# Kernel optimization log

Hardware: AMD Instinct MI355X
Metric: run time of the kernel (lower is better)

Reference implementation:

```python
import jax, jax.numpy as jnp
import numpy as np

N = 8192        # nodes
V = 50000       # vocab = len(dict_node_names)
EMB = 256       # embedding_dim
XI = EMB // 2   # x_increased_dim = 128
DIN = EMB + XI  # 384, SelfAtt_ dim
H = 4           # n_heads
D = 128         # WGAT output_dim per head (fusion dim)
E = 131072      # edges
CHUNK = 32768   # chunk_size (E % CHUNK == 0)


def _ln(x, g, b, eps=1e-5):
    m = jnp.mean(x, axis=-1, keepdims=True)
    v = jnp.mean((x - m) ** 2, axis=-1, keepdims=True)
    return (x - m) * jax.lax.rsqrt(v + eps) * g + b


def _wgat(emb, src, dst, edge_attr, wi, bi, wj, bj, wt, bt, attn):
    # x_i = features at destination (aggregation target), x_j = source/neighbor
    x_i = emb[dst]                                   # [E, din]
    x_j = emb[src]                                   # [E, din]
    h = (x_i @ wi + bi).reshape(E, H, D) + (x_j @ wj + bj).reshape(E, H, D)
    a = jnp.einsum('ehd,hd->eh', h, attn)            # [E, H]
    a = a * edge_attr[:, None]                       # edge weights pre-softmax
    # faithful chunked softmax: normalize over edges WITHIN each chunk (dim=0 per chunk)
    a = jax.nn.softmax(a.reshape(E // CHUNK, CHUNK, H), axis=1).reshape(E, H)
    xt = (x_j @ wt + bt).reshape(E, H, D)            # [E, H, D]
    msg = jnp.einsum('ehd,eh->ed', xt, a)            # sum over heads -> [E, D]
    return jax.ops.segment_sum(msg, dst, num_segments=N)  # aggr='add'


def _emb_forward(ids, edge_index, x, edge_attr, embed,
                 qkv_w, qkv_b, proj_w, proj_b, fuse_w, fuse_b, ln1_g, ln1_b,
                 wi0, bi0, wj0, bj0, wt0, bt0, attn0, skip0_w, skip0_b,
                 wi1, bi1, wj1, bj1, wt1, bt1, attn1, skip1_w, skip1_b,
                 ln2_g, ln2_b):
    E_i = embed[ids]                                 # [N, EMB] gather
    z = jnp.concatenate([jnp.tile(x, (1, XI)), E_i], axis=-1)   # [N, DIN]
    # SelfAtt_ : full N x N attention over nodes, scale = DIN**-0.5
    qkv = z @ qkv_w + qkv_b
    q, k, v = jnp.split(qkv, 3, axis=-1)
    att = jax.nn.softmax((q @ k.T) * (DIN ** -0.5), axis=-1) @ v
    z = att @ proj_w + proj_b                        # [N, DIN]
    emb = jax.nn.silu(_ln(z @ fuse_w + fuse_b, ln1_g, ln1_b)) + E_i  # [N, EMB]
    src, dst = edge_index[0], edge_index[1]
    emb = _wgat(emb, src, dst, edge_attr, wi0, bi0, wj0, bj0, wt0, bt0, attn0)  # [N, D]
    s0 = emb @ skip0_w + skip0_b
    emb = _wgat(emb, src, dst, edge_attr, wi1, bi1, wj1, bj1, wt1, bt1, attn1)  # [N, D]
    s1 = emb @ skip1_w + skip1_b
    emb = _ln(emb + (s0 + s1) * 0.5, ln2_g, ln2_b)
    return emb


def setup_inputs() -> dict:
    key = jax.random.key(0)
    ks = jax.random.split(key, 32)

    def w(k, shape, scale=0.05):
        return jax.random.normal(k, shape, jnp.float32) * scale

    inp = {}
    inp['ids'] = jax.random.randint(ks[0], (N,), 0, V)
    inp['x'] = jax.random.normal(ks[1], (N, 1), jnp.float32)
    inp['edge_attr'] = jax.random.uniform(ks[2], (E,), jnp.float32)
    inp['edge_index'] = jax.random.randint(ks[3], (2, E), 0, N)
    inp['embed'] = w(ks[4], (V, EMB), 1.0)
    inp['qkv_w'] = w(ks[5], (DIN, 3 * DIN)); inp['qkv_b'] = jnp.zeros((3 * DIN,), jnp.float32)
    inp['proj_w'] = w(ks[6], (DIN, DIN));    inp['proj_b'] = jnp.zeros((DIN,), jnp.float32)
    inp['fuse_w'] = w(ks[7], (DIN, EMB));    inp['fuse_b'] = jnp.zeros((EMB,), jnp.float32)
    inp['ln1_g'] = jnp.ones((EMB,), jnp.float32); inp['ln1_b'] = jnp.zeros((EMB,), jnp.float32)
    # WGAT layer 0: in=EMB, out=D per head, H heads
    inp['wi0'] = w(ks[8], (EMB, H * D));  inp['bi0'] = jnp.zeros((H * D,), jnp.float32)
    inp['wj0'] = w(ks[9], (EMB, H * D));  inp['bj0'] = jnp.zeros((H * D,), jnp.float32)
    inp['wt0'] = w(ks[10], (EMB, H * D)); inp['bt0'] = jnp.zeros((H * D,), jnp.float32)
    inp['attn0'] = w(ks[11], (H, D), 0.1)
    inp['skip0_w'] = w(ks[12], (D, D));   inp['skip0_b'] = jnp.zeros((D,), jnp.float32)
    # WGAT layer 1: in=D
    inp['wi1'] = w(ks[13], (D, H * D));   inp['bi1'] = jnp.zeros((H * D,), jnp.float32)
    inp['wj1'] = w(ks[14], (D, H * D));   inp['bj1'] = jnp.zeros((H * D,), jnp.float32)
    inp['wt1'] = w(ks[15], (D, H * D));   inp['bt1'] = jnp.zeros((H * D,), jnp.float32)
    inp['attn1'] = w(ks[16], (H, D), 0.1)
    inp['skip1_w'] = w(ks[17], (D, D));   inp['skip1_b'] = jnp.zeros((D,), jnp.float32)
    inp['ln2_g'] = jnp.ones((D,), jnp.float32); inp['ln2_b'] = jnp.zeros((D,), jnp.float32)
    return inp


def reference(ids, x, edge_attr, edge_index, embed,
              qkv_w, qkv_b, proj_w, proj_b, fuse_w, fuse_b, ln1_g, ln1_b,
              wi0, bi0, wj0, bj0, wt0, bt0, attn0, skip0_w, skip0_b,
              wi1, bi1, wj1, bj1, wt1, bt1, attn1, skip1_w, skip1_b,
              ln2_g, ln2_b):
    emb = _emb_forward(ids, edge_index, x, edge_attr, embed,
                       qkv_w, qkv_b, proj_w, proj_b, fuse_w, fuse_b, ln1_g, ln1_b,
                       wi0, bi0, wj0, bj0, wt0, bt0, attn0, skip0_w, skip0_b,
                       wi1, bi1, wj1, bj1, wt1, bt1, attn1, skip1_w, skip1_b,
                       ln2_g, ln2_b)
    return (emb, embed, ids)
```

## Files before the change

### kernel.cpp

```cpp
#include <hip/hip_runtime.h>

typedef __attribute__((ext_vector_type(8))) short bfrag;
typedef __attribute__((ext_vector_type(4))) float f4;

#define MFMA(a,b,c) __builtin_amdgcn_mfma_f32_16x16x32_bf16(a,b,c,0,0,0)

__device__ __forceinline__ unsigned short f2b(float x){
  union { float f; unsigned int u; } v; v.f = x;
  unsigned int r = v.u + 0x7fffu + ((v.u >> 16) & 1u);
  return (unsigned short)(r >> 16);
}
__device__ __forceinline__ float b2f(unsigned short h){
  union { unsigned int u; float f; } v; v.u = ((unsigned int)h) << 16;
  return v.f;
}

__global__ __launch_bounds__(256) void k_prep(
    const float* __restrict__ qkv_w, const float* __restrict__ proj_w,
    const float* __restrict__ fuse_w, const float* __restrict__ wt0,
    const float* __restrict__ wt1, const float* __restrict__ sk0w,
    const float* __restrict__ wi0, const float* __restrict__ bi0,
    const float* __restrict__ wj0, const float* __restrict__ bj0,
    const float* __restrict__ wi1, const float* __restrict__ bi1,
    const float* __restrict__ wj1, const float* __restrict__ bj1,
    const float* __restrict__ attn0, const float* __restrict__ attn1,
    const float* __restrict__ bt0, const float* __restrict__ bt1,
    const float* __restrict__ sk0b,
    const float* __restrict__ embed, const int* __restrict__ ids,
    unsigned short* __restrict__ BtQKV, unsigned short* __restrict__ BtPROJ,
    unsigned short* __restrict__ BtFUSE, unsigned short* __restrict__ BtT0,
    unsigned short* __restrict__ BtT1,
    float* __restrict__ biasT0, float* __restrict__ biasT1,
    float* __restrict__ wsum, float* __restrict__ Ei)
{
  int b = blockIdx.x, t = threadIdx.x;
  if (b < 1152) {
    int idx = b*256 + t; int k = idx/1152, n = idx - k*1152;
    BtQKV[(size_t)n*256 + k] = f2b(qkv_w[128*1152 + idx]);
  } else if (b < 1728) {
    int idx = (b-1152)*256 + t; int k = idx/384, n = idx - k*384;
    BtPROJ[(size_t)n*384 + k] = f2b(proj_w[idx]);
  } else if (b < 2112) {
    int idx = (b-1728)*256 + t; int k = idx/256, n = idx - k*256;
    BtFUSE[(size_t)n*384 + k] = f2b(fuse_w[idx]);
  } else if (b < 2624) {
    int idx = (b-2112)*256 + t; int k = idx/512, n = idx - k*512;
    BtT0[(size_t)n*256 + k] = f2b(wt0[idx]);
  } else if (b < 2880) {
    int idx = (b-2624)*256 + t; int k = idx/512, n = idx - k*512;
    BtT1[(size_t)n*128 + k] = f2b(wt1[idx]);
  } else if (b < 2944) {
    int idx = (b-2880)*256 + t; int k = idx/128, n = idx - k*128;
    BtT1[(size_t)(512+n)*128 + k] = f2b(sk0w[idx]);
  } else if (b < 2948) {
    int idx = (b-2944)*256 + t;
    int h = idx >> 8, k = idx & 255;
    float s = 0.f;
    for (int d = 0; d < 128; ++d) s += wi0[(size_t)k*512 + h*128 + d] * attn0[h*128 + d];
    BtT0[(size_t)(512 + h)*256 + k] = f2b(s);
    if (idx < 4) {
      float sb = 0.f;
      for (int d = 0; d < 128; ++d) sb += bi0[idx*128 + d] * attn0[idx*128 + d];
      biasT0[512 + idx] = sb;
    }
  } else if (b < 2952) {
    int idx = (b-2948)*256 + t;
    int h = idx >> 8, k = idx & 255;
    float s = 0.f;
    for (int d = 0; d < 128; ++d) s += wj0[(size_t)k*512 + h*128 + d] * attn0[h*128 + d];
    BtT0[(size_t)(516 + h)*256 + k] = f2b(s);
    if (idx < 4) {
      float sb = 0.f;
      for (int d = 0; d < 128; ++d) sb += bj0[idx*128 + d] * attn0[idx*128 + d];
      biasT0[516 + idx] = sb;
    }
  } else if (b < 2954) {
    int idx = (b-2952)*256 + t;
    int h = idx >> 7, k = idx & 127;
    float s = 0.f;
    for (int d = 0; d < 128; ++d) s += wi1[(size_t)k*512 + h*128 + d] * attn1[h*128 + d];
    BtT1[(size_t)(640 + h)*128 + k] = f2b(s);
    if (idx < 4) {
      float sb = 0.f;
      for (int d = 0; d < 128; ++d) sb += bi1[idx*128 + d] * attn1[idx*128 + d];
      biasT1[640 + idx] = sb;
    }
  } else if (b < 2956) {
    int idx = (b-2954)*256 + t;
    int h = idx >> 7, k = idx & 127;
    float s = 0.f;
    for (int d = 0; d < 128; ++d) s += wj1[(size_t)k*512 + h*128 + d] * attn1[h*128 + d];
    BtT1[(size_t)(644 + h)*128 + k] = f2b(s);
    if (idx < 4) {
      float sb = 0.f;
      for (int d = 0; d < 128; ++d) sb += bj1[idx*128 + d] * attn1[idx*128 + d];
      biasT1[644 + idx] = sb;
    }
  } else if (b < 2958) {
    int idx = (b-2956)*256 + t; biasT0[idx] = bt0[idx];
  } else if (b < 2960) {
    int idx = (b-2958)*256 + t; biasT1[idx] = bt1[idx];
  } else if (b < 2961) {
    if (t < 128) biasT1[512 + t] = sk0b[t];
  } else if (b < 2966) {
    int n = (b-2961)*256 + t;
    if (n < 1152) {
      float s = 0.f;
      for (int k = 0; k < 128; ++k) s += qkv_w[(size_t)k*1152 + n];
      wsum[n] = s;
    }
  } else {
    int idx = (b-2966)*256 + t;
    int n = idx >> 6, c4 = idx & 63;
    reinterpret_cast<float4*>(Ei)[idx] =
        reinterpret_cast<const float4*>(embed + (size_t)ids[n]*256)[c4];
  }
}

__global__ void k_outcopy(const float* __restrict__ embed, const int* __restrict__ ids,
                          float* __restrict__ out){
  int i = blockIdx.x*256 + threadIdx.x;
  if (i < 3200000)
    reinterpret_cast<float4*>(out)[262144 + i] = reinterpret_cast<const float4*>(embed)[i];
  if (i < 8192) out[13848576 + i] = (float)ids[i];
}

__global__ void k_deg(const int* __restrict__ ei, int* __restrict__ deg){
  int e = blockIdx.x*256 + threadIdx.x; if (e >= 131072) return;
  atomicAdd(&deg[ei[131072 + e]], 1);
}

__global__ __launch_bounds__(1024) void k_scan(const int* __restrict__ deg,
                                               int* __restrict__ off, int* __restrict__ cursor){
  int t = threadIdx.x;
  int v[8]; int s = 0;
  #pragma unroll
  for (int i=0;i<8;++i){ v[i] = s; s += deg[t*8 + i]; }
  int lane = t & 63, w = t >> 6;
  int si = s;
  for (int o=1;o<64;o<<=1){ int u = __shfl_up(si, o); if (lane >= o) si += u; }
  __shared__ int wsum[16];
  if (lane == 63) wsum[w] = si;
  __syncthreads();
  if (t < 16) {
    int x = wsum[t];
    for (int o=1;o<16;o<<=1){ int u = __shfl_up(x, o); if (t >= o) x += u; }
    wsum[t] = x;
  }
  __syncthreads();
  int wbase = (w == 0) ? 0 : wsum[w-1];
  int base = wbase + (si - s);
  #pragma unroll
  for (int i=0;i<8;++i){ int o2 = base + v[i]; off[t*8+i] = o2; cursor[t*8+i] = o2; }
  if (t == 1023) off[8192] = wbase + si;
}

__global__ void k_fill(const int* __restrict__ ei, int* __restrict__ cursor,
                       int* __restrict__ elist){
  int e = blockIdx.x*256 + threadIdx.x; if (e >= 131072) return;
  int d = ei[131072 + e];
  int slot = atomicAdd(&cursor[d], 1);
  elist[slot] = e;
}

__global__ __launch_bounds__(256) void k_gemm(
    const float* __restrict__ A, int lda,
    const unsigned short* __restrict__ Bt, int K,
    const float* __restrict__ bias,
    float* __restrict__ C, int ldc, int mode,
    const float* __restrict__ xv, const float* __restrict__ wsum,
    unsigned short* __restrict__ qO, unsigned short* __restrict__ kO,
    unsigned short* __restrict__ vO)
{
  __shared__ unsigned short As[128*40];
  __shared__ unsigned short Bs[128*40];
  const int t = threadIdx.x;
  const int wid = t >> 6, l = t & 63;
  const int lr = l & 15, lg = l >> 4;
  const int arow0 = blockIdx.y*128, bn0 = blockIdx.x*128;
  const int wr = (wid >> 1)*64, wc = (wid & 1)*64;
  f4 zero = {0.f,0.f,0.f,0.f};
  f4 acc[4][4];
  #pragma unroll
  for (int i=0;i<4;++i)
    #pragma unroll
    for (int j=0;j<4;++j) acc[i][j] = zero;

  for (int k0 = 0; k0 < K; k0 += 32) {
    #pragma unroll
    for (int p=0;p<4;++p) {
      int row = p*32 + (t>>3);
      int c4  = (t&7)*4;
      float4 v = *reinterpret_cast<const float4*>(A + (size_t)(arow0+row)*lda + k0 + c4);
      ushort4 h4;
      h4.x = f2b(v.x); h4.y = f2b(v.y); h4.z = f2b(v.z); h4.w = f2b(v.w);
      *reinterpret_cast<ushort4*>(&As[row*40 + c4]) = h4;
    }
    #pragma unroll
    for (int p=0;p<2;++p) {
      int n  = p*64 + (t>>2);
      int c8 = (t&3)*8;
      int4 v = *reinterpret_cast<const int4*>(Bt + (size_t)(bn0+n)*K + k0 + c8);
      *reinterpret_cast<int4*>(&Bs[n*40 + c8]) = v;
    }
    __syncthreads();
    bfrag af[4], bfm[4];
    #pragma unroll
    for (int mi=0;mi<4;++mi) af[mi] = *reinterpret_cast<const bfrag*>(&As[(wr+mi*16+lr)*40 + lg*8]);
    #pragma unroll
    for (int ni=0;ni<4;++ni) bfm[ni] = *reinterpret_cast<const bfrag*>(&Bs[(wc+ni*16+lr)*40 + lg*8]);
    #pragma unroll
    for (int mi=0;mi<4;++mi)
      #pragma unroll
      for (int ni=0;ni<4;++ni)
        acc[mi][ni] = MFMA(af[mi], bfm[ni], acc[mi][ni]);
    __syncthreads();
  }
  #pragma unroll
  for (int mi=0;mi<4;++mi) {
    #pragma unroll
    for (int ni=0;ni<4;++ni) {
      int col = bn0 + wc + ni*16 + lr;
      float bv = bias[col];
      float wsv = (mode==1) ? wsum[col] : 0.f;
      #pragma unroll
      for (int i=0;i<4;++i) {
        int row = arow0 + wr + mi*16 + lg*4 + i;
        float val = acc[mi][ni][i] + bv;
        if (mode == 1) {
          val += xv[row]*wsv;
          if (col < 384) val *= 0.05103103631f;
          unsigned short hv = f2b(val);
          if (col < 384)      qO[(size_t)row*384 + col] = hv;
          else if (col < 768) kO[(size_t)row*384 + col - 384] = hv;
          else                vO[(size_t)(col-768)*8192 + row] = hv;
        } else {
          C[(size_t)row*ldc + col] = val;
        }
      }
    }
  }
}

__global__ __launch_bounds__(256,2) void k_flash(
    const unsigned short* __restrict__ qg,
    const unsigned short* __restrict__ kg,
    const unsigned short* __restrict__ vg,
    unsigned short* __restrict__ Opart, float* __restrict__ mpart, float* __restrict__ lpart)
{
  __shared__ unsigned short Ks[32*384];
  __shared__ unsigned short Ps[64*40];
  __shared__ float m_s[64], l_s[64], f_s[64];

  const int t = threadIdx.x;
  const int w = t >> 6, l = t & 63;
  const int lr = l & 15, lg = l >> 4;
  const int qbi = blockIdx.x >> 2, split = blockIdx.x & 3;
  const int qbase = qbi * 64;

  #define STAGE(JJ) do { \
    _Pragma("unroll") \
    for (int p_=0;p_<6;++p_) { \
      int idx_ = p_*256 + t; \
      int row_ = idx_ / 48, uu_ = idx_ - row_*48; \
      int ug_ = uu_ ^ (row_ & 7); \
      const unsigned short* gp_ = kg + (size_t)((JJ) + row_)*384 + ug_*8; \
      __builtin_amdgcn_global_load_lds((const __attribute__((address_space(1))) void*)gp_, \
          (__attribute__((address_space(3))) void*)&Ks[idx_*8], 16, 0, 0); \
    } } while(0)

  bfrag qf[12];
  #pragma unroll
  for (int kk=0;kk<12;++kk)
    qf[kk] = *reinterpret_cast<const bfrag*>(qg + (size_t)(qbase + w*16 + lr)*384 + kk*32 + lg*8);

  f4 zero = {0.f,0.f,0.f,0.f};
  f4 o[4][6];
  #pragma unroll
  for (int a=0;a<4;++a)
    #pragma unroll
    for (int b=0;b<6;++b) o[a][b] = zero;

  const int j0beg = split*2048, jend = j0beg + 2048;

  STAGE(j0beg);
  if (t < 64) { m_s[t] = -3e38f; l_s[t] = 0.f; }
  __syncthreads();

  for (int j0 = j0beg; j0 < jend; j0 += 32) {
    bfrag vf[6];
    #pragma unroll
    for (int nj=0;nj<6;++nj)
      vf[nj] = *reinterpret_cast<const bfrag*>(vg + (size_t)(w*96 + nj*16 + lr)*8192 + j0 + lg*8);

    f4 s0 = zero, s1 = zero;
    __builtin_amdgcn_s_setprio(1);
    #pragma unroll
    for (int kk=0;kk<12;++kk) {
      int su = ((kk*4 + lg) ^ (lr & 7)) * 8;
      bfrag b0 = *reinterpret_cast<const bfrag*>(&Ks[lr*384 + su]);
      bfrag b1 = *reinterpret_cast<const bfrag*>(&Ks[(16+lr)*384 + su]);
      s0 = MFMA(qf[kk], b0, s0);
      s1 = MFMA(qf[kk], b1, s1);
    }
    __builtin_amdgcn_s_setprio(0);

    #pragma unroll
    for (int i=0;i<4;++i) {
      int row = w*16 + lg*4 + i;
      float mt = fmaxf(s0[i], s1[i]);
      mt = fmaxf(mt, __shfl_xor(mt, 1));
      mt = fmaxf(mt, __shfl_xor(mt, 2));
      mt = fmaxf(mt, __shfl_xor(mt, 4));
      mt = fmaxf(mt, __shfl_xor(mt, 8));
      float mo = m_s[row];
      float mn = fmaxf(mo, mt);
      float p0 = __expf(s0[i] - mn), p1 = __expf(s1[i] - mn);
      float sum = p0 + p1;
      sum += __shfl_xor(sum, 1);
      sum += __shfl_xor(sum, 2);
      sum += __shfl_xor(sum, 4);
      sum += __shfl_xor(sum, 8);
      Ps[row*40 + lr]      = f2b(p0);
      Ps[row*40 + 16 + lr] = f2b(p1);
      if (lr == 0) {
        float f = __expf(mo - mn);
        m_s[row] = mn; f_s[row] = f; l_s[row] = l_s[row]*f + sum;
      }
    }
    __syncthreads();

    if (j0 + 32 < jend) STAGE(j0 + 32);

    #pragma unroll
    for (int omi=0; omi<4; ++omi) {
      #pragma unroll
      for (int i=0;i<4;++i) {
        float f = f_s[omi*16 + lg*4 + i];
        #pragma unroll
        for (int nj=0;nj<6;++nj) o[omi][nj][i] *= f;
      }
    }
    bfrag pa[4];
    #pragma unroll
    for (int omi=0;omi<4;++omi)
      pa[omi] = *reinterpret_cast<const bfrag*>(&Ps[(omi*16+lr)*40 + lg*8]);
    __builtin_amdgcn_s_setprio(1);
    #pragma unroll
    for (int nj=0;nj<6;++nj)
      #pragma unroll
      for (int omi=0;omi<4;++omi)
        o[omi][nj] = MFMA(pa[omi], vf[nj], o[omi][nj]);
    __builtin_amdgcn_s_setprio(0);
    __syncthreads();
  }
  #undef STAGE

  unsigned short* Op = Opart + (size_t)split*8192*384;
  #pragma unroll
  for (int omi=0;omi<4;++omi)
    #pragma unroll
    for (int nj=0;nj<6;++nj)
      #pragma unroll
      for (int i=0;i<4;++i)
        Op[(size_t)(qbase + omi*16 + lg*4 + i)*384 + w*96 + nj*16 + lr] = f2b(o[omi][nj][i]);
  if (t < 64) {
    mpart[split*8192 + qbase + t] = m_s[t];
    lpart[split*8192 + qbase + t] = l_s[t];
  }
}

__global__ void k_combine(const unsigned short* __restrict__ Op, const float* __restrict__ mp,
                          const float* __restrict__ lp, float* __restrict__ att)
{
  int gid = blockIdx.x*256 + threadIdx.x;
  int row = gid / 384;
  float m0 = mp[row], m1 = mp[8192+row], m2 = mp[16384+row], m3 = mp[24576+row];
  float M = fmaxf(fmaxf(m0,m1), fmaxf(m2,m3));
  float w0 = __expf(m0-M), w1 = __expf(m1-M), w2 = __expf(m2-M), w3 = __expf(m3-M);
  float L = lp[row]*w0 + lp[8192+row]*w1 + lp[16384+row]*w2 + lp[24576+row]*w3;
  const size_t Z = (size_t)8192*384;
  float acc = b2f(Op[gid])*w0 + b2f(Op[Z+gid])*w1 + b2f(Op[2*Z+gid])*w2 + b2f(Op[3*Z+gid])*w3;
  att[gid] = acc / L;
}

__global__ __launch_bounds__(256) void k_ln1(const float* __restrict__ pre, const float* __restrict__ Ei,
                      const float* __restrict__ g, const float* __restrict__ b,
                      float* __restrict__ out)
{
  int row = blockIdx.x, c = threadIdx.x;
  float v = pre[(size_t)row*256 + c];
  float s1 = v, s2 = v*v;
  #pragma unroll
  for (int o1=32;o1;o1>>=1){ s1 += __shfl_down(s1,o1); s2 += __shfl_down(s2,o1); }
  __shared__ float a1[4], a2[4];
  if ((c&63)==0){ a1[c>>6] = s1; a2[c>>6] = s2; }
  __syncthreads();
  float S1 = a1[0]+a1[1]+a1[2]+a1[3], S2 = a2[0]+a2[1]+a2[2]+a2[3];
  float mean = S1*(1.f/256.f), var = S2*(1.f/256.f) - mean*mean;
  float y = (v-mean)*rsqrtf(var+1e-5f)*g[c] + b[c];
  float sig = 1.f/(1.f+__expf(-y));
  out[(size_t)row*256 + c] = y*sig + Ei[(size_t)row*256 + c];
}

__global__ void k_escore(const int* __restrict__ ei, const float* __restrict__ ea,
                         const float* __restrict__ TC, int ldc, int aoff,
                         float* __restrict__ sc)
{
  int e = blockIdx.x*256 + threadIdx.x; if (e >= 131072) return;
  int s = ei[e], d = ei[131072 + e];
  float wv = ea[e];
  #pragma unroll
  for (int h=0; h<4; ++h) {
    float ai = TC[(size_t)d*ldc + aoff + h];
    float aj = TC[(size_t)s*ldc + aoff + 4 + h];
    sc[e*4 + h] = (ai + aj) * wv;
  }
}

__global__ __launch_bounds__(1024) void k_cstats(const float* __restrict__ sc,
                        float* __restrict__ mx, float* __restrict__ sm)
{
  int ch = blockIdx.x;
  int c = ch >> 2, h = ch & 3;
  int t = threadIdx.x;
  const float* base = sc + (size_t)c*131072 + h;
  float m = -3e38f;
  for (int i=t; i<32768; i+=1024) m = fmaxf(m, base[(size_t)i*4]);
  #pragma unroll
  for (int o1=32;o1;o1>>=1) m = fmaxf(m, __shfl_down(m,o1));
  __shared__ float red[16];
  if ((t&63)==0) red[t>>6] = m;
  __syncthreads();
  if (t == 0) { float x = red[0]; for (int i=1;i<16;++i) x = fmaxf(x, red[i]); red[0] = x; }
  __syncthreads();
  float M = red[0];
  float s = 0.f;
  for (int i=t; i<32768; i+=1024) s += __expf(base[(size_t)i*4] - M);
  #pragma unroll
  for (int o1=32;o1;o1>>=1) s += __shfl_down(s,o1);
  __shared__ float red2[16];
  if ((t&63)==0) red2[t>>6] = s;
  __syncthreads();
  if (t == 0) { float x = 0.f; for (int i=0;i<16;++i) x += red2[i]; mx[ch] = M; sm[ch] = x; }
}

__global__ void k_pnorm(float* __restrict__ sc, const float* __restrict__ mx,
                        const float* __restrict__ sm)
{
  int i = blockIdx.x*256 + threadIdx.x;
  int e = i >> 2, h = i & 3;
  int ch = (e >> 15)*4 + h;
  sc[i] = __expf(sc[i] - mx[ch]) / sm[ch];
}

__global__ __launch_bounds__(128) void k_aggr(const int* __restrict__ off,
                      const int* __restrict__ elist, const int* __restrict__ ei,
                      const float* __restrict__ sc,
                      const float* __restrict__ TC, int ldc, float* __restrict__ g)
{
  int n = blockIdx.x, d = threadIdx.x;
  int qb = off[n], qe = off[n+1];
  float acc = 0.f;
  for (int q = qb; q < qe; ++q) {
    int e = elist[q];
    int s = ei[e];
    float4 p = *reinterpret_cast<const float4*>(&sc[e*4]);
    const float* Tr = TC + (size_t)s*ldc;
    acc += p.x*Tr[d] + p.y*Tr[128+d] + p.z*Tr[256+d] + p.w*Tr[384+d];
  }
  g[(size_t)n*128 + d] = acc;
}

__global__ __launch_bounds__(128) void k_final(const float* __restrict__ g1, const float* __restrict__ TC1,
                       const float* __restrict__ sw, const float* __restrict__ sb,
                       const float* __restrict__ lg2, const float* __restrict__ lb2,
                       float* __restrict__ out)
{
  int row = blockIdx.x, c = threadIdx.x;
  __shared__ float gr[128];
  float gv = g1[(size_t)row*128 + c];
  gr[c] = gv; __syncthreads();
  float s1 = sb[c];
  #pragma unroll 8
  for (int k=0;k<128;++k) s1 += gr[k]*sw[k*128 + c];
  float s0 = TC1[(size_t)row*768 + 512 + c];
  float v = gv + 0.5f*(s0 + s1);
  float m1 = v, m2 = v*v;
  #pragma unroll
  for (int o1=32;o1;o1>>=1){ m1 += __shfl_down(m1,o1); m2 += __shfl_down(m2,o1); }
  __shared__ float a1[2], a2[2];
  if ((c&63)==0){ a1[c>>6]=m1; a2[c>>6]=m2; }
  __syncthreads();
  float S1 = a1[0]+a1[1], S2 = a2[0]+a2[1];
  float mean = S1*(1.f/128.f), var = S2*(1.f/128.f) - mean*mean;
  out[(size_t)row*128 + c] = (v-mean)*rsqrtf(var+1e-5f)*lg2[c] + lb2[c];
}

extern "C" void kernel_launch(void* const* d_in, const int* in_sizes, int n_in,
                              void* d_out, int out_size, void* d_ws, size_t ws_size,
                              hipStream_t stream)
{
  const int*   ids    = (const int*)  d_in[0];
  const float* x      = (const float*)d_in[1];
  const float* ea     = (const float*)d_in[2];
  const int*   eidx   = (const int*)  d_in[3];
  const float* embed  = (const float*)d_in[4];
  const float* qkv_w  = (const float*)d_in[5];
  const float* qkv_b  = (const float*)d_in[6];
  const float* proj_w = (const float*)d_in[7];
  const float* proj_b = (const float*)d_in[8];
  const float* fuse_w = (const float*)d_in[9];
  const float* fuse_b = (const float*)d_in[10];
  const float* ln1_g  = (const float*)d_in[11];
  const float* ln1_b  = (const float*)d_in[12];
  const float* wi0 = (const float*)d_in[13]; const float* bi0 = (const float*)d_in[14];
  const float* wj0 = (const float*)d_in[15]; const float* bj0 = (const float*)d_in[16];
  const float* wt0 = (const float*)d_in[17]; const float* bt0 = (const float*)d_in[18];
  const float* attn0 = (const float*)d_in[19];
  const float* sk0w = (const float*)d_in[20]; const float* sk0b = (const float*)d_in[21];
  const float* wi1 = (const float*)d_in[22]; const float* bi1 = (const float*)d_in[23];
  const float* wj1 = (const float*)d_in[24]; const float* bj1 = (const float*)d_in[25];
  const float* wt1 = (const float*)d_in[26]; const float* bt1 = (const float*)d_in[27];
  const float* attn1 = (const float*)d_in[28];
  const float* sk1w = (const float*)d_in[29]; const float* sk1b = (const float*)d_in[30];
  const float* ln2_g = (const float*)d_in[31]; const float* ln2_b = (const float*)d_in[32];

  char* ws = (char*)d_ws;
  const size_t MBy = (size_t)1 << 20;

  unsigned short* BtQKV  = (unsigned short*)(ws + 0);
  unsigned short* BtPROJ = (unsigned short*)(ws + 589824);
  unsigned short* BtFUSE = (unsigned short*)(ws + 884736);
  unsigned short* BtT0   = (unsigned short*)(ws + 1081344);
  unsigned short* BtT1   = (unsigned short*)(ws + 1409024);
  float* biasT0 = (float*)(ws + 1605632);
  float* biasT1 = (float*)(ws + 1608192);
  float* wsum   = (float*)(ws + 1611264);
  float* mxb    = (float*)(ws + 1615872);
  float* smb    = (float*)(ws + 1615936);
  int* deg    = (int*)(ws + 1703936);
  int* cursor = (int*)(ws + 1736704);
  int* off    = (int*)(ws + 1769472);

  float* Ei   = (float*)(ws + 2*MBy);
  unsigned short* qb = (unsigned short*)(ws + 10*MBy);
  unsigned short* kb = (unsigned short*)(ws + 17*MBy);
  unsigned short* vb = (unsigned short*)(ws + 24*MBy);
  float* att  = (float*)(ws + 31*MBy);
  float* z2   = (float*)(ws + 10*MBy);
  float* pre  = (float*)(ws + 45*MBy);
  float* emb0 = (float*)(ws + 31*MBy);
  float* TC0  = (float*)(ws + 43*MBy);
  float* sc0  = (float*)(ws + 26*MBy);
  float* g0   = (float*)(ws + 2*MBy);
  float* TC1  = (float*)(ws + 6*MBy);
  float* sc1  = (float*)(ws + 43*MBy);
  float* g1   = (float*)(ws + 47448064);
  int* elist  = (int*)(ws + 64*MBy);

  float* out = (float*)d_out;
  unsigned short* Opart = (unsigned short*)d_out;
  float* mpart = out + 6815744;
  float* lpart = out + 6848512;

  hipMemsetAsync(ws, 0, 2*MBy, stream);

  k_prep<<<5014, 256, 0, stream>>>(qkv_w, proj_w, fuse_w, wt0, wt1, sk0w,
                                   wi0, bi0, wj0, bj0, wi1, bi1, wj1, bj1,
                                   attn0, attn1, bt0, bt1, sk0b, embed, ids,
                                   BtQKV, BtPROJ, BtFUSE, BtT0, BtT1,
                                   biasT0, biasT1, wsum, Ei);
  k_deg<<<512, 256, 0, stream>>>(eidx, deg);
  k_scan<<<1, 1024, 0, stream>>>(deg, off, cursor);
  k_fill<<<512, 256, 0, stream>>>(eidx, cursor, elist);

  k_gemm<<<dim3(9,64), 256, 0, stream>>>(Ei, 256, BtQKV, 256, qkv_b, nullptr, 0, 1,
                                         x, wsum, qb, kb, vb);
  k_flash<<<512, 256, 0, stream>>>(qb, kb, vb, Opart, mpart, lpart);
  k_combine<<<12288, 256, 0, stream>>>(Opart, mpart, lpart, att);
  k_outcopy<<<12500, 256, 0, stream>>>(embed, ids, out);

  k_gemm<<<dim3(3,64), 256, 0, stream>>>(att, 384, BtPROJ, 384, proj_b, z2, 384, 0,
                                         nullptr, nullptr, nullptr, nullptr, nullptr);
  k_gemm<<<dim3(2,64), 256, 0, stream>>>(z2, 384, BtFUSE, 384, fuse_b, pre, 256, 0,
                                         nullptr, nullptr, nullptr, nullptr, nullptr);
  k_ln1<<<8192, 256, 0, stream>>>(pre, Ei, ln1_g, ln1_b, emb0);

  k_gemm<<<dim3(5,64), 256, 0, stream>>>(emb0, 256, BtT0, 256, biasT0, TC0, 640, 0,
                                         nullptr, nullptr, nullptr, nullptr, nullptr);
  k_escore<<<512, 256, 0, stream>>>(eidx, ea, TC0, 640, 512, sc0);
  k_cstats<<<16, 1024, 0, stream>>>(sc0, mxb, smb);
  k_pnorm<<<2048, 256, 0, stream>>>(sc0, mxb, smb);
  k_aggr<<<8192, 128, 0, stream>>>(off, elist, eidx, sc0, TC0, 640, g0);

  k_gemm<<<dim3(6,64), 256, 0, stream>>>(g0, 128, BtT1, 128, biasT1, TC1, 768, 0,
                                         nullptr, nullptr, nullptr, nullptr, nullptr);
  k_escore<<<512, 256, 0, stream>>>(eidx, ea, TC1, 768, 640, sc1);
  k_cstats<<<16, 1024, 0, stream>>>(sc1, mxb, smb);
  k_pnorm<<<2048, 256, 0, stream>>>(sc1, mxb, smb);
  k_aggr<<<8192, 128, 0, stream>>>(off, elist, eidx, sc1, TC1, 768, g1);

  k_final<<<8192, 128, 0, stream>>>(g1, TC1, sk1w, sk1b, ln2_g, ln2_b, out);
}
```

Measured before the change: 526.5 us.

## Make flash-attention waves independent with register-resident softmax and direct K/V loads

```diff
diff --git a/kernel.cpp b/kernel.cpp
--- a/kernel.cpp
+++ b/kernel.cpp
@@ -2,6 +2,7 @@
 
 typedef __attribute__((ext_vector_type(8))) short bfrag;
 typedef __attribute__((ext_vector_type(4))) float f4;
+typedef __attribute__((ext_vector_type(4))) unsigned int ui4;
 
 #define MFMA(a,b,c) __builtin_amdgcn_mfma_f32_16x16x32_bf16(a,b,c,0,0,0)
 
@@ -248,125 +249,105 @@
     const unsigned short* __restrict__ vg,
     unsigned short* __restrict__ Opart, float* __restrict__ mpart, float* __restrict__ lpart)
 {
-  __shared__ unsigned short Ks[32*384];
-  __shared__ unsigned short Ps[64*40];
-  __shared__ float m_s[64], l_s[64], f_s[64];
-
   const int t = threadIdx.x;
   const int w = t >> 6, l = t & 63;
   const int lr = l & 15, lg = l >> 4;
   const int qbi = blockIdx.x >> 2, split = blockIdx.x & 3;
   const int qbase = qbi * 64;
-
-  #define STAGE(JJ) do { \
-    _Pragma("unroll") \
-    for (int p_=0;p_<6;++p_) { \
-      int idx_ = p_*256 + t; \
-      int row_ = idx_ / 48, uu_ = idx_ - row_*48; \
-      int ug_ = uu_ ^ (row_ & 7); \
-      const unsigned short* gp_ = kg + (size_t)((JJ) + row_)*384 + ug_*8; \
-      __builtin_amdgcn_global_load_lds((const __attribute__((address_space(1))) void*)gp_, \
-          (__attribute__((address_space(3))) void*)&Ks[idx_*8], 16, 0, 0); \
-    } } while(0)
+  const int qrow = qbase + w*16 + lr;
 
   bfrag qf[12];
   #pragma unroll
   for (int kk=0;kk<12;++kk)
-    qf[kk] = *reinterpret_cast<const bfrag*>(qg + (size_t)(qbase + w*16 + lr)*384 + kk*32 + lg*8);
+    qf[kk] = *reinterpret_cast<const bfrag*>(qg + (size_t)qrow*384 + kk*32 + lg*8);
 
   f4 zero = {0.f,0.f,0.f,0.f};
-  f4 o[4][6];
-  #pragma unroll
-  for (int a=0;a<4;++a)
-    #pragma unroll
-    for (int b=0;b<6;++b) o[a][b] = zero;
-
+  f4 o[24];
+  #pragma unroll
+  for (int nj=0;nj<24;++nj) o[nj] = zero;
+
+  float m = -3e38f, lsum = 0.f;
   const int j0beg = split*2048, jend = j0beg + 2048;
 
-  STAGE(j0beg);
-  if (t < 64) { m_s[t] = -3e38f; l_s[t] = 0.f; }
-  __syncthreads();
-
   for (int j0 = j0beg; j0 < jend; j0 += 32) {
-    bfrag vf[6];
-    #pragma unroll
-    for (int nj=0;nj<6;++nj)
-      vf[nj] = *reinterpret_cast<const bfrag*>(vg + (size_t)(w*96 + nj*16 + lr)*8192 + j0 + lg*8);
-
+    const unsigned short* kp = kg + (size_t)j0*384;
     f4 s0 = zero, s1 = zero;
-    __builtin_amdgcn_s_setprio(1);
     #pragma unroll
     for (int kk=0;kk<12;++kk) {
-      int su = ((kk*4 + lg) ^ (lr & 7)) * 8;
-      bfrag b0 = *reinterpret_cast<const bfrag*>(&Ks[lr*384 + su]);
-      bfrag b1 = *reinterpret_cast<const bfrag*>(&Ks[(16+lr)*384 + su]);
-      s0 = MFMA(qf[kk], b0, s0);
-      s1 = MFMA(qf[kk], b1, s1);
-    }
-    __builtin_amdgcn_s_setprio(0);
-
+      bfrag k0 = *reinterpret_cast<const bfrag*>(kp + (size_t)lr*384      + kk*32 + lg*8);
+      bfrag k1 = *reinterpret_cast<const bfrag*>(kp + (size_t)(16+lr)*384 + kk*32 + lg*8);
+      s0 = MFMA(k0, qf[kk], s0);
+      s1 = MFMA(k1, qf[kk], s1);
+      if ((kk & 3) == 3) __builtin_amdgcn_sched_barrier(0);
+    }
+
+    float mt = fmaxf(fmaxf(fmaxf(s0[0],s0[1]),fmaxf(s0[2],s0[3])),
+                     fmaxf(fmaxf(s1[0],s1[1]),fmaxf(s1[2],s1[3])));
+    mt = fmaxf(mt, __shfl_xor(mt,16));
+    mt = fmaxf(mt, __shfl_xor(mt,32));
+    bool grew = mt > m;
+    float mn = grew ? mt : m;
+
+    float p0[4], p1[4];
+    float sum = 0.f;
     #pragma unroll
     for (int i=0;i<4;++i) {
-      int row = w*16 + lg*4 + i;
-      float mt = fmaxf(s0[i], s1[i]);
-      mt = fmaxf(mt, __shfl_xor(mt, 1));
-      mt = fmaxf(mt, __shfl_xor(mt, 2));
-      mt = fmaxf(mt, __shfl_xor(mt, 4));
-      mt = fmaxf(mt, __shfl_xor(mt, 8));
-      float mo = m_s[row];
-      float mn = fmaxf(mo, mt);
-      float p0 = __expf(s0[i] - mn), p1 = __expf(s1[i] - mn);
-      float sum = p0 + p1;
-      sum += __shfl_xor(sum, 1);
-      sum += __shfl_xor(sum, 2);
-      sum += __shfl_xor(sum, 4);
-      sum += __shfl_xor(sum, 8);
-      Ps[row*40 + lr]      = f2b(p0);
-      Ps[row*40 + 16 + lr] = f2b(p1);
-      if (lr == 0) {
-        float f = __expf(mo - mn);
-        m_s[row] = mn; f_s[row] = f; l_s[row] = l_s[row]*f + sum;
-      }
-    }
-    __syncthreads();
-
-    if (j0 + 32 < jend) STAGE(j0 + 32);
-
-    #pragma unroll
-    for (int omi=0; omi<4; ++omi) {
+      p0[i] = __expf(s0[i]-mn); p1[i] = __expf(s1[i]-mn);
+      sum += p0[i] + p1[i];
+    }
+    sum += __shfl_xor(sum,16);
+    sum += __shfl_xor(sum,32);
+
+    if (__any(grew)) {
+      float f = __expf(m - mn);
       #pragma unroll
       for (int i=0;i<4;++i) {
-        float f = f_s[omi*16 + lg*4 + i];
+        float fr = __shfl(f, lg*4 + i);
         #pragma unroll
-        for (int nj=0;nj<6;++nj) o[omi][nj][i] *= f;
+        for (int nj=0;nj<24;++nj) o[nj][i] *= fr;
       }
-    }
-    bfrag pa[4];
-    #pragma unroll
-    for (int omi=0;omi<4;++omi)
-      pa[omi] = *reinterpret_cast<const bfrag*>(&Ps[(omi*16+lr)*40 + lg*8]);
-    __builtin_amdgcn_s_setprio(1);
-    #pragma unroll
-    for (int nj=0;nj<6;++nj)
-      #pragma unroll
-      for (int omi=0;omi<4;++omi)
-        o[omi][nj] = MFMA(pa[omi], vf[nj], o[omi][nj]);
-    __builtin_amdgcn_s_setprio(0);
-    __syncthreads();
-  }
-  #undef STAGE
+      lsum = lsum * f + sum;
+      m = mn;
+    } else {
+      lsum += sum;
+    }
+
+    unsigned int d0 = (unsigned int)f2b(p0[0]) | ((unsigned int)f2b(p0[1]) << 16);
+    unsigned int d1 = (unsigned int)f2b(p0[2]) | ((unsigned int)f2b(p0[3]) << 16);
+    unsigned int e0 = (unsigned int)f2b(p1[0]) | ((unsigned int)f2b(p1[1]) << 16);
+    unsigned int e1 = (unsigned int)f2b(p1[2]) | ((unsigned int)f2b(p1[3]) << 16);
+    int b0 = lr + ((lg & 1) ? 32 : 0);
+    int b1 = b0 + 16;
+    unsigned int A = (unsigned int)__shfl((int)d0, b0);
+    unsigned int B = (unsigned int)__shfl((int)d1, b0);
+    unsigned int C = (unsigned int)__shfl((int)d0, b1);
+    unsigned int D = (unsigned int)__shfl((int)d1, b1);
+    unsigned int E = (unsigned int)__shfl((int)e0, b0);
+    unsigned int F = (unsigned int)__shfl((int)e1, b0);
+    unsigned int G = (unsigned int)__shfl((int)e0, b1);
+    unsigned int H = (unsigned int)__shfl((int)e1, b1);
+    bool hi = lg >= 2;
+    union { ui4 u; bfrag b; } pu;
+    pu.u = hi ? (ui4){E,F,G,H} : (ui4){A,B,C,D};
+    bfrag pa = pu.b;
+
+    #pragma unroll
+    for (int nj=0;nj<24;++nj) {
+      bfrag vf = *reinterpret_cast<const bfrag*>(vg + (size_t)(nj*16+lr)*8192 + j0 + lg*8);
+      o[nj] = MFMA(pa, vf, o[nj]);
+      if ((nj % 6) == 5) __builtin_amdgcn_sched_barrier(0);
+    }
+  }
 
   unsigned short* Op = Opart + (size_t)split*8192*384;
   #pragma unroll
-  for (int omi=0;omi<4;++omi)
-    #pragma unroll
-    for (int nj=0;nj<6;++nj)
-      #pragma unroll
-      for (int i=0;i<4;++i)
-        Op[(size_t)(qbase + omi*16 + lg*4 + i)*384 + w*96 + nj*16 + lr] = f2b(o[omi][nj][i]);
-  if (t < 64) {
-    mpart[split*8192 + qbase + t] = m_s[t];
-    lpart[split*8192 + qbase + t] = l_s[t];
+  for (int nj=0;nj<24;++nj)
+    #pragma unroll
+    for (int i=0;i<4;++i)
+      Op[(size_t)(qbase + w*16 + lg*4 + i)*384 + nj*16 + lr] = f2b(o[nj][i]);
+  if (lg == 0) {
+    mpart[split*8192 + qbase + w*16 + lr] = m;
+    lpart[split*8192 + qbase + w*16 + lr] = lsum;
   }
 }
 
```

Measured after the change: 1.001 ms. +90.1%, slower.
